# Kernel tuning notes

Hardware: AMD Instinct MI355X
Metric: run time of the kernel (lower is better)

## Reference

```python
import jax, jax.numpy as jnp
import numpy as np

HIDDEN = 1024
HEADS = 16
HEAD_DIM = HIDDEN // HEADS
B, S = 2, 2048


def setup_inputs() -> dict:
    key = jax.random.key(0)
    k1, k2, k3 = jax.random.split(key, 3)
    scale_in = 1.0 / np.sqrt(HIDDEN)
    x = jax.random.normal(k1, (B, S, HIDDEN), dtype=jnp.float32)
    wqkv_w = jax.random.normal(k2, (3 * HIDDEN, HIDDEN), dtype=jnp.float32) * scale_in
    wo_w = jax.random.normal(k3, (HIDDEN, HIDDEN), dtype=jnp.float32) * scale_in
    wo_b = jnp.zeros((HIDDEN,), dtype=jnp.float32)
    return {"x": x, "wqkv_w": wqkv_w, "wo_w": wo_w, "wo_b": wo_b}


def reference(x, wqkv_w, wo_w, wo_b):
    b, s, d = x.shape
    h, hd = HEADS, HEAD_DIM
    sm_scale = hd ** (-0.5)
    # QKV projection (torch Linear: x @ W^T), then chunk into q,k,v
    qkv = jnp.einsum('bsd,ed->bse', x, wqkv_w)  # [b, s, 3d]
    q, k, v = jnp.split(qkv, 3, axis=-1)
    # [b, h, s, hd]
    q = q.reshape(b, s, h, hd).transpose(0, 2, 1, 3)
    k = k.reshape(b, s, h, hd).transpose(0, 2, 1, 3)
    v = v.reshape(b, s, h, hd).transpose(0, 2, 1, 3)
    # raw scores, then causal mask (mask applied BEFORE scaling, as in source;
    # -inf * scale == -inf so math matches softmax(score*scale) with mask)
    scores = jnp.einsum('bhqe,bhke->bhqk', q, k)
    causal = jnp.tril(jnp.ones((s, s), dtype=bool))
    scores = jnp.where(causal[None, None, :, :], scores, -jnp.inf)
    weights = jax.nn.softmax(scores * sm_scale, axis=-1)
    # dropout p=0.0 (eval) -> identity
    out = jnp.einsum('bhqk,bhke->bhqe', weights, v)
    out = out.transpose(0, 2, 1, 3).reshape(b, s, h * hd)
    y = jnp.einsum('bsd,ed->bse', out, wo_w) + wo_b
    return (y, k, v)
```

## Files before the change

### kernel.cpp

```cpp
#include <hip/hip_runtime.h>
#include <cstdint>
#include <cstddef>


using bf16x8 = __attribute__((ext_vector_type(8))) __bf16;
using f32x4  = __attribute__((ext_vector_type(4))) float;
using u16    = unsigned short;

#define SOFT_SCALE 0.1803368801111244f

__device__ __forceinline__ u16 f2bf(float f) {
  union { float f; uint32_t u; } a; a.f = f;
  uint32_t r = a.u + 0x7fffu + ((a.u >> 16) & 1u);
  return (u16)(r >> 16);
}

__device__ __forceinline__ bf16x8 ldfrag(const u16* p) {
  return *reinterpret_cast<const bf16x8*>(p);
}

__device__ __forceinline__ void gload_lds16(const void* g, void* l) {
  __builtin_amdgcn_global_load_lds((const __attribute__((address_space(1))) void*)g,
                                   (__attribute__((address_space(3))) void*)l,
                                   16, 0, 0);
}

__global__ void cvt_all(const float* __restrict__ x, const float* __restrict__ wqkv,
                        const float* __restrict__ wo,
                        u16* __restrict__ xb, u16* __restrict__ wqkvb, u16* __restrict__ wob) {
  int i = blockIdx.x * blockDim.x + threadIdx.x;
  int stride = gridDim.x * blockDim.x;
  for (; i < 2097152; i += stride) {
    const float* src; u16* dst; int j;
    if (i < 1048576)      { src = x;    dst = xb;    j = i; }
    else if (i < 1835008) { src = wqkv; dst = wqkvb; j = i - 1048576; }
    else                  { src = wo;   dst = wob;   j = i - 1835008; }
    float4 v = reinterpret_cast<const float4*>(src)[j];
    ushort4 o;
    o.x = f2bf(v.x); o.y = f2bf(v.y); o.z = f2bf(v.z); o.w = f2bf(v.w);
    reinterpret_cast<ushort4*>(dst)[j] = o;
  }
}

__global__ __launch_bounds__(512, 2) void qkv_gemm_kernel(
    const u16* __restrict__ Xb, const u16* __restrict__ Wb,
    u16* __restrict__ Qws, u16* __restrict__ Kws, u16* __restrict__ Vtws,
    float* __restrict__ out) {
  extern __shared__ char smem[];

  const int tid = threadIdx.x, lane = tid & 63, wid = tid >> 6;
  const int wr = wid >> 2, wc = wid & 3;
  const int fq = lane >> 4, fr = lane & 15;

  const int wg = (blockIdx.x & 7) * 24 + (blockIdx.x >> 3);
  const int bm = wg / 12, bn = wg % 12;
  const int m0 = bm * 256, n0 = bn * 256;

  const char* Ab = (const char*)Xb + (size_t)m0 * 2048;
  const char* Bb = (const char*)Wb + (size_t)n0 * 2048;

  f32x4 acc[8][4] = {};

  auto stage = [&](int t, int cc) {
    char* As = smem + cc * 32768;
    char* Bs = smem + 65536 + cc * 32768;
#pragma unroll
    for (int f = 0; f < 4; ++f) {
      int lin = (f * 512 + tid) * 16;
      int row = lin >> 7;
      int col = (lin & 127) ^ ((row & 7) << 4);
      gload_lds16(Ab + (size_t)row * 2048 + t * 128 + col, As + lin);
      gload_lds16(Bb + (size_t)row * 2048 + t * 128 + col, Bs + lin);
    }
  };

  stage(0, 0);
  int cur = 0;
  for (int t = 0; t < 16; ++t) {
    if (t < 15) {
      stage(t + 1, cur ^ 1);
      asm volatile("s_waitcnt vmcnt(8)" ::: "memory");
    } else {
      asm volatile("s_waitcnt vmcnt(0)" ::: "memory");
    }
    __builtin_amdgcn_s_barrier();
    __builtin_amdgcn_sched_barrier(0);

    const char* As = smem + cur * 32768;
    const char* Bs = smem + 65536 + cur * 32768;

#pragma unroll
    for (int ks = 0; ks < 2; ++ks) {
      bf16x8 af[8];
#pragma unroll
      for (int m = 0; m < 8; ++m) {
        int row = wr * 128 + m * 16 + fr;
        int col = (ks * 64 + fq * 16) ^ ((row & 7) << 4);
        af[m] = *(const bf16x8*)(As + row * 128 + col);
      }
#pragma unroll
      for (int nh = 0; nh < 2; ++nh) {
        int row0 = wc * 64 + (nh * 2) * 16 + fr;
        int col0 = (ks * 64 + fq * 16) ^ ((row0 & 7) << 4);
        bf16x8 bf0 = *(const bf16x8*)(Bs + row0 * 128 + col0);
        int row1 = wc * 64 + (nh * 2 + 1) * 16 + fr;
        int col1 = (ks * 64 + fq * 16) ^ ((row1 & 7) << 4);
        bf16x8 bf1 = *(const bf16x8*)(Bs + row1 * 128 + col1);
        __builtin_amdgcn_s_setprio(1);
#pragma unroll
        for (int m = 0; m < 8; ++m) {
          acc[m][nh * 2]     = __builtin_amdgcn_mfma_f32_16x16x32_bf16(af[m], bf0, acc[m][nh * 2], 0, 0, 0);
          acc[m][nh * 2 + 1] = __builtin_amdgcn_mfma_f32_16x16x32_bf16(af[m], bf1, acc[m][nh * 2 + 1], 0, 0, 0);
        }
        __builtin_amdgcn_s_setprio(0);
      }
    }
    asm volatile("s_waitcnt lgkmcnt(0)" ::: "memory");
    __builtin_amdgcn_s_barrier();
    cur ^= 1;
  }

  const int sect = n0 >> 10;
  const int nn0 = (n0 & 1023) + wc * 64;
  const int mbase = m0 + wr * 128;
#pragma unroll
  for (int m = 0; m < 8; ++m)
#pragma unroll
    for (int n = 0; n < 4; ++n) {
      int mB = mbase + m * 16 + fq * 4;
      int ncol = nn0 + n * 16 + fr;
      int b = mB >> 11, s0 = mB & 2047;
      int h = ncol >> 6, hd = ncol & 63;
      size_t base = (((size_t)b * 16 + h) * 2048 + s0) * 64 + hd;
      float v0 = acc[m][n][0], v1 = acc[m][n][1], v2 = acc[m][n][2], v3 = acc[m][n][3];
      if (sect == 0) {
        Qws[base] = f2bf(v0); Qws[base + 64] = f2bf(v1);
        Qws[base + 128] = f2bf(v2); Qws[base + 192] = f2bf(v3);
      } else if (sect == 1) {
        Kws[base] = f2bf(v0); Kws[base + 64] = f2bf(v1);
        Kws[base + 128] = f2bf(v2); Kws[base + 192] = f2bf(v3);
        out[4194304 + base] = v0; out[4194304 + base + 64] = v1;
        out[4194304 + base + 128] = v2; out[4194304 + base + 192] = v3;
      } else {
        out[8388608 + base] = v0; out[8388608 + base + 64] = v1;
        out[8388608 + base + 128] = v2; out[8388608 + base + 192] = v3;
        size_t tt = ((size_t)(b * 16 + h) * 64 + hd) * 2048 + s0;
        ushort4 pk; pk.x = f2bf(v0); pk.y = f2bf(v1); pk.z = f2bf(v2); pk.w = f2bf(v3);
        *reinterpret_cast<ushort4*>(Vtws + tt) = pk;
      }
    }
}

__device__ __forceinline__ void gemm128_core(const u16* __restrict__ A,
                                             const u16* __restrict__ B,
                                             int m0, int n0, int K,
                                             u16* As, u16* Bs, f32x4 acc[4][4]) {
  const int tid  = threadIdx.x;
  const int lane = tid & 63;
  const int wid  = tid >> 6;
  const int wr = wid >> 1, wc = wid & 1;
  const int fq = lane >> 4, fr = lane & 15;

  for (int kb = 0; kb < K; kb += 32) {
#pragma unroll
    for (int j = 0; j < 2; ++j) {
      int lin = (j * 256 + tid) * 16;
      int row = lin >> 6;
      int rb  = lin & 63;
      gload_lds16((const char*)(A + (size_t)(m0 + row) * K + kb) + rb, (char*)As + lin);
      gload_lds16((const char*)(B + (size_t)(n0 + row) * K + kb) + rb, (char*)Bs + lin);
    }
    __syncthreads();

    bf16x8 av[4], bv[4];
#pragma unroll
    for (int i = 0; i < 4; ++i) av[i] = ldfrag(As + (wr * 64 + i * 16 + fr) * 32 + fq * 8);
#pragma unroll
    for (int j = 0; j < 4; ++j) bv[j] = ldfrag(Bs + (wc * 64 + j * 16 + fr) * 32 + fq * 8);
    __builtin_amdgcn_s_setprio(1);
#pragma unroll
    for (int i = 0; i < 4; ++i)
#pragma unroll
      for (int j = 0; j < 4; ++j)
        acc[i][j] = __builtin_amdgcn_mfma_f32_16x16x32_bf16(av[i], bv[j], acc[i][j], 0, 0, 0);
    __builtin_amdgcn_s_setprio(0);
    __syncthreads();
  }
}

__global__ __launch_bounds__(256) void attn_kernel(
    const u16* __restrict__ Qw, const u16* __restrict__ Kw,
    const u16* __restrict__ Vtw, u16* __restrict__ Ow) {
  __shared__ u16 Ks[2][64 * 64];
  __shared__ u16 Vs[2][64 * 64];
  __shared__ u16 Ps[4 * 16 * 64];

  const int tid = threadIdx.x, lane = tid & 63, wid = tid >> 6;
  const int fq = lane >> 4, fr = lane & 15;
  const int bh = blockIdx.x & 31;
  const int qb = 31 - (blockIdx.x >> 5);
  const int b = bh >> 4, h = bh & 15;
  const int q0 = qb * 64;

  const u16* Qbase  = Qw  + (size_t)bh * 2048 * 64;
  const u16* Kbase  = Kw  + (size_t)bh * 2048 * 64;
  const char* VtBase = (const char*)(Vtw + (size_t)bh * 64 * 2048);
  u16* Psw = Ps + wid * 1024;

#pragma unroll
  for (int f = 0; f < 2; ++f) {
    int lin = (f * 256 + tid) * 16;
    int row = lin >> 7;
    int logical = lin ^ ((row & 7) << 4);
    gload_lds16((const char*)Kbase + logical, (char*)Ks[0] + lin);
    gload_lds16(VtBase + (size_t)row * 4096 + (logical & 127), (char*)Vs[0] + lin);
  }

  const int qrow = q0 + wid * 16 + fr;
  bf16x8 qa0 = ldfrag(Qbase + (size_t)qrow * 64 + fq * 8);
  bf16x8 qa1 = ldfrag(Qbase + (size_t)qrow * 64 + 32 + fq * 8);

  float ssum[4] = {0.f, 0.f, 0.f, 0.f};
  f32x4 accO[4] = {};

  int cur = 0;
  for (int kb = 0; kb <= qb; ++kb) {
    __syncthreads();

    if (kb < qb) {
      const char* kg = (const char*)(Kbase + (size_t)(kb + 1) * 64 * 64);
#pragma unroll
      for (int f = 0; f < 2; ++f) {
        int lin = (f * 256 + tid) * 16;
        int row = lin >> 7;
        int logical = lin ^ ((row & 7) << 4);
        gload_lds16(kg + logical, (char*)Ks[cur ^ 1] + lin);
        gload_lds16(VtBase + (size_t)row * 4096 + (size_t)(kb + 1) * 128 + (logical & 127),
                    (char*)Vs[cur ^ 1] + lin);
      }
    }

    const u16* Kc = Ks[cur];
    const u16* Vc = Vs[cur];

    f32x4 sfr[4];
    __builtin_amdgcn_s_setprio(1);
#pragma unroll
    for (int n = 0; n < 4; ++n) {
      int krow = n * 16 + fr;
      bf16x8 kf0 = ldfrag(Kc + krow * 64 + ((fq * 8)      ^ ((krow & 7) << 3)));
      bf16x8 kf1 = ldfrag(Kc + krow * 64 + ((fq * 8 + 32) ^ ((krow & 7) << 3)));
      f32x4 z = {};
      z = __builtin_amdgcn_mfma_f32_16x16x32_bf16(qa0, kf0, z, 0, 0, 0);
      z = __builtin_amdgcn_mfma_f32_16x16x32_bf16(qa1, kf1, z, 0, 0, 0);
      sfr[n] = z;
    }
    __builtin_amdgcn_s_setprio(0);

#pragma unroll
    for (int n = 0; n < 4; ++n) {
      int kvcol = kb * 64 + n * 16 + fr;
#pragma unroll
      for (int r = 0; r < 4; ++r) {
        float t = sfr[n][r] * SOFT_SCALE;
        if (kb == qb) {
          int qr = q0 + wid * 16 + fq * 4 + r;
          if (kvcol > qr) t = -1e30f;
        }
        float p = exp2f(t);
        ssum[r] += p;
        int prow = fq * 4 + r;
        Psw[prow * 64 + ((n * 16 + fr) ^ ((prow & 7) << 3))] = f2bf(p);
      }
    }

    bf16x8 pa0 = ldfrag(Psw + fr * 64 + ((fq * 8)      ^ ((fr & 7) << 3)));
    bf16x8 pa1 = ldfrag(Psw + fr * 64 + ((fq * 8 + 32) ^ ((fr & 7) << 3)));
    __builtin_amdgcn_s_setprio(1);
#pragma unroll
    for (int nh = 0; nh < 4; ++nh) {
      int vrow = nh * 16 + fr;
      bf16x8 vb0 = ldfrag(Vc + vrow * 64 + ((fq * 8)      ^ ((vrow & 7) << 3)));
      bf16x8 vb1 = ldfrag(Vc + vrow * 64 + ((fq * 8 + 32) ^ ((vrow & 7) << 3)));
      accO[nh] = __builtin_amdgcn_mfma_f32_16x16x32_bf16(pa0, vb0, accO[nh], 0, 0, 0);
      accO[nh] = __builtin_amdgcn_mfma_f32_16x16x32_bf16(pa1, vb1, accO[nh], 0, 0, 0);
    }
    __builtin_amdgcn_s_setprio(0);
    cur ^= 1;
  }

#pragma unroll
  for (int r = 0; r < 4; ++r) {
#pragma unroll
    for (int d = 1; d < 16; d <<= 1) ssum[r] += __shfl_xor(ssum[r], d);
    ssum[r] = 1.0f / ssum[r];
  }

#pragma unroll
  for (int nh = 0; nh < 4; ++nh)
#pragma unroll
    for (int r = 0; r < 4; ++r) {
      float o = accO[nh][r] * ssum[r];
      int qr = q0 + wid * 16 + fq * 4 + r;
      Ow[((size_t)b * 2048 + qr) * 1024 + h * 64 + nh * 16 + fr] = f2bf(o);
    }
}

__global__ __launch_bounds__(256) void proj_gemm_kernel(
    const u16* __restrict__ Ob, const u16* __restrict__ Wob,
    const float* __restrict__ bias, float* __restrict__ out) {
  __shared__ u16 As[128 * 32];
  __shared__ u16 Bs[128 * 32];
  const int NB = 8;
  int m0 = (blockIdx.x / NB) * 128, n0 = (blockIdx.x % NB) * 128;
  f32x4 acc[4][4] = {};
  gemm128_core(Ob, Wob, m0, n0, 1024, As, Bs, acc);

  const int lane = threadIdx.x & 63, wid = threadIdx.x >> 6;
  const int wr = wid >> 1, wc = wid & 1, fq = lane >> 4, fr = lane & 15;
#pragma unroll
  for (int i = 0; i < 4; ++i)
#pragma unroll
    for (int j = 0; j < 4; ++j)
#pragma unroll
      for (int r = 0; r < 4; ++r) {
        int m = m0 + wr * 64 + i * 16 + fq * 4 + r;
        int n = n0 + wc * 64 + j * 16 + fr;
        out[(size_t)m * 1024 + n] = acc[i][j][r] + bias[n];
      }
}

extern "C" void kernel_launch(void* const* d_in, const int* in_sizes, int n_in,
                              void* d_out, int out_size, void* d_ws, size_t ws_size,
                              hipStream_t stream) {
  const float* x    = (const float*)d_in[0];
  const float* wqkv = (const float*)d_in[1];
  const float* wo   = (const float*)d_in[2];
  const float* wo_b = (const float*)d_in[3];
  float* out = (float*)d_out;

  u16* xb    = (u16*)d_ws;
  u16* wqkvb = xb    + 4194304;
  u16* wob   = wqkvb + 3145728;
  u16* q_ws  = wob   + 1048576;
  u16* k_ws  = q_ws  + 4194304;
  u16* vt_ws = k_ws  + 4194304;
  u16* o_ws  = vt_ws + 4194304;

  static bool attr_set = false;
  if (!attr_set) {
    hipFuncSetAttribute((const void*)qkv_gemm_kernel,
                        hipFuncAttributeMaxDynamicSharedMemorySize, 131072);
    attr_set = true;
  }

  cvt_all<<<2048, 256, 0, stream>>>(x, wqkv, wo, xb, wqkvb, wob);
  qkv_gemm_kernel<<<192, 512, 131072, stream>>>(xb, wqkvb, q_ws, k_ws, vt_ws, out);
  attn_kernel<<<32 * 32, 256, 0, stream>>>(q_ws, k_ws, vt_ws, o_ws);
  proj_gemm_kernel<<<32 * 8, 256, 0, stream>>>(o_ws, wob, wo_b, out);
}
```

Measured before the change: 123.9 us.

## Compute transposed S tile with 32-wide KV blocks to store P without shuffles

The attention kernel now processes KV in 32-column tiles instead of 64. Swapping the MFMA operand order computes S transposed, so each lane holds four consecutive KV entries for one query row. Those probabilities are packed with v_cvt_pk_bf16_f32 and written to LDS as 8-byte vector stores, and a single P fragment feeds the PV MFMA. The row-sum reduction shrinks to two cross-lane shuffles. The cost is twice as many loop iterations and barriers per block, plus smaller K/V tiles loaded each iteration.

```diff
diff --git a/kernel.cpp b/kernel.cpp
--- a/kernel.cpp
+++ b/kernel.cpp
@@ -23,6 +23,12 @@
   __builtin_amdgcn_global_load_lds((const __attribute__((address_space(1))) void*)g,
                                    (__attribute__((address_space(3))) void*)l,
                                    16, 0, 0);
+}
+
+__device__ __forceinline__ uint32_t cvt_pk_bf16(float a, float b) {
+  uint32_t r;
+  asm("v_cvt_pk_bf16_f32 %0, %1, %2" : "=v"(r) : "v"(a), "v"(b));
+  return r;
 }
 
 __global__ void cvt_all(const float* __restrict__ x, const float* __restrict__ wqkv,
@@ -191,9 +197,9 @@
 __global__ __launch_bounds__(256) void attn_kernel(
     const u16* __restrict__ Qw, const u16* __restrict__ Kw,
     const u16* __restrict__ Vtw, u16* __restrict__ Ow) {
-  __shared__ u16 Ks[2][64 * 64];
-  __shared__ u16 Vs[2][64 * 64];
-  __shared__ u16 Ps[4 * 16 * 64];
+  __shared__ u16 Ks[2][32 * 64];
+  __shared__ u16 Vs[2][64 * 32];
+  __shared__ u16 Ps[4 * 16 * 32];
 
   const int tid = threadIdx.x, lane = tid & 63, wid = tid >> 6;
   const int fq = lane >> 4, fr = lane & 15;
@@ -203,104 +209,98 @@
   const int q0 = qb * 64;
 
   const u16* Qbase  = Qw  + (size_t)bh * 2048 * 64;
-  const u16* Kbase  = Kw  + (size_t)bh * 2048 * 64;
+  const char* Kbase = (const char*)(Kw + (size_t)bh * 2048 * 64);
   const char* VtBase = (const char*)(Vtw + (size_t)bh * 64 * 2048);
-  u16* Psw = Ps + wid * 1024;
-
-#pragma unroll
-  for (int f = 0; f < 2; ++f) {
-    int lin = (f * 256 + tid) * 16;
-    int row = lin >> 7;
-    int logical = lin ^ ((row & 7) << 4);
-    gload_lds16((const char*)Kbase + logical, (char*)Ks[0] + lin);
-    gload_lds16(VtBase + (size_t)row * 4096 + (logical & 127), (char*)Vs[0] + lin);
-  }
+  u16* Psw = Ps + wid * 512;
+
+  auto stageKV = [&](int kb32, int cc) {
+    int lin = tid * 16;
+    int krow = lin >> 7;
+    int kcol = (lin & 127) ^ ((krow & 7) << 4);
+    gload_lds16(Kbase + (size_t)kb32 * 4096 + krow * 128 + kcol, (char*)Ks[cc] + lin);
+    int vrow = lin >> 6;
+    int vcol = lin & 63;
+    gload_lds16(VtBase + (size_t)vrow * 4096 + kb32 * 64 + vcol, (char*)Vs[cc] + lin);
+  };
+
+  stageKV(0, 0);
 
   const int qrow = q0 + wid * 16 + fr;
   bf16x8 qa0 = ldfrag(Qbase + (size_t)qrow * 64 + fq * 8);
   bf16x8 qa1 = ldfrag(Qbase + (size_t)qrow * 64 + 32 + fq * 8);
 
-  float ssum[4] = {0.f, 0.f, 0.f, 0.f};
+  float ssum = 0.f;
   f32x4 accO[4] = {};
 
+  const int ktiles = 2 * qb + 2;
   int cur = 0;
-  for (int kb = 0; kb <= qb; ++kb) {
+  for (int kb = 0; kb < ktiles; ++kb) {
     __syncthreads();
 
-    if (kb < qb) {
-      const char* kg = (const char*)(Kbase + (size_t)(kb + 1) * 64 * 64);
-#pragma unroll
-      for (int f = 0; f < 2; ++f) {
-        int lin = (f * 256 + tid) * 16;
-        int row = lin >> 7;
-        int logical = lin ^ ((row & 7) << 4);
-        gload_lds16(kg + logical, (char*)Ks[cur ^ 1] + lin);
-        gload_lds16(VtBase + (size_t)row * 4096 + (size_t)(kb + 1) * 128 + (logical & 127),
-                    (char*)Vs[cur ^ 1] + lin);
-      }
-    }
+    if (kb + 1 < ktiles) stageKV(kb + 1, cur ^ 1);
 
     const u16* Kc = Ks[cur];
     const u16* Vc = Vs[cur];
 
-    f32x4 sfr[4];
+    f32x4 sfr[2];
     __builtin_amdgcn_s_setprio(1);
 #pragma unroll
-    for (int n = 0; n < 4; ++n) {
+    for (int n = 0; n < 2; ++n) {
       int krow = n * 16 + fr;
       bf16x8 kf0 = ldfrag(Kc + krow * 64 + ((fq * 8)      ^ ((krow & 7) << 3)));
       bf16x8 kf1 = ldfrag(Kc + krow * 64 + ((fq * 8 + 32) ^ ((krow & 7) << 3)));
       f32x4 z = {};
-      z = __builtin_amdgcn_mfma_f32_16x16x32_bf16(qa0, kf0, z, 0, 0, 0);
-      z = __builtin_amdgcn_mfma_f32_16x16x32_bf16(qa1, kf1, z, 0, 0, 0);
+      z = __builtin_amdgcn_mfma_f32_16x16x32_bf16(kf0, qa0, z, 0, 0, 0);
+      z = __builtin_amdgcn_mfma_f32_16x16x32_bf16(kf1, qa1, z, 0, 0, 0);
       sfr[n] = z;
     }
     __builtin_amdgcn_s_setprio(0);
 
-#pragma unroll
-    for (int n = 0; n < 4; ++n) {
-      int kvcol = kb * 64 + n * 16 + fr;
+    float p[2][4];
+#pragma unroll
+    for (int n = 0; n < 2; ++n)
 #pragma unroll
       for (int r = 0; r < 4; ++r) {
         float t = sfr[n][r] * SOFT_SCALE;
-        if (kb == qb) {
-          int qr = q0 + wid * 16 + fq * 4 + r;
-          if (kvcol > qr) t = -1e30f;
+        if (kb >= 2 * qb) {
+          int kvg = kb * 32 + n * 16 + fq * 4 + r;
+          if (kvg > qrow) t = -1e30f;
         }
-        float p = exp2f(t);
-        ssum[r] += p;
-        int prow = fq * 4 + r;
-        Psw[prow * 64 + ((n * 16 + fr) ^ ((prow & 7) << 3))] = f2bf(p);
-      }
-    }
-
-    bf16x8 pa0 = ldfrag(Psw + fr * 64 + ((fq * 8)      ^ ((fr & 7) << 3)));
-    bf16x8 pa1 = ldfrag(Psw + fr * 64 + ((fq * 8 + 32) ^ ((fr & 7) << 3)));
+        p[n][r] = exp2f(t);
+        ssum += p[n][r];
+      }
+
+#pragma unroll
+    for (int n = 0; n < 2; ++n) {
+      uint2 w;
+      w.x = cvt_pk_bf16(p[n][0], p[n][1]);
+      w.y = cvt_pk_bf16(p[n][2], p[n][3]);
+      *reinterpret_cast<uint2*>((char*)Psw + fr * 64 + n * 32 + fq * 8) = w;
+    }
+
+    bf16x8 pa = ldfrag(Psw + fr * 32 + fq * 8);
     __builtin_amdgcn_s_setprio(1);
 #pragma unroll
     for (int nh = 0; nh < 4; ++nh) {
-      int vrow = nh * 16 + fr;
-      bf16x8 vb0 = ldfrag(Vc + vrow * 64 + ((fq * 8)      ^ ((vrow & 7) << 3)));
-      bf16x8 vb1 = ldfrag(Vc + vrow * 64 + ((fq * 8 + 32) ^ ((vrow & 7) << 3)));
-      accO[nh] = __builtin_amdgcn_mfma_f32_16x16x32_bf16(pa0, vb0, accO[nh], 0, 0, 0);
-      accO[nh] = __builtin_amdgcn_mfma_f32_16x16x32_bf16(pa1, vb1, accO[nh], 0, 0, 0);
+      bf16x8 vb = ldfrag(Vc + (nh * 16 + fr) * 32 + fq * 8);
+      accO[nh] = __builtin_amdgcn_mfma_f32_16x16x32_bf16(pa, vb, accO[nh], 0, 0, 0);
     }
     __builtin_amdgcn_s_setprio(0);
     cur ^= 1;
   }
 
-#pragma unroll
-  for (int r = 0; r < 4; ++r) {
-#pragma unroll
-    for (int d = 1; d < 16; d <<= 1) ssum[r] += __shfl_xor(ssum[r], d);
-    ssum[r] = 1.0f / ssum[r];
-  }
+  ssum += __shfl_xor(ssum, 16);
+  ssum += __shfl_xor(ssum, 32);
+  float inv = 1.0f / ssum;
+  float invq[4];
+#pragma unroll
+  for (int r = 0; r < 4; ++r) invq[r] = __shfl(inv, fq * 4 + r);
 
 #pragma unroll
   for (int nh = 0; nh < 4; ++nh)
 #pragma unroll
     for (int r = 0; r < 4; ++r) {
-      float o = accO[nh][r] * ssum[r];
+      float o = accO[nh][r] * invq[r];
       int qr = q0 + wid * 16 + fq * 4 + r;
       Ow[((size_t)b * 2048 + qr) * 1024 + h * 64 + nh * 16 + fr] = f2bf(o);
     }
```

Result: slower. 143.1 us (+15.5%).
